# Performance work log

Measured on AMD Instinct MI355X. Metric: run time of the kernel, lower is better.

## Reference

```python
import jax, jax.numpy as jnp
import numpy as np

NUM_EXPERTS = 8
TOP_K = 2
HIDDEN = 1024
INTER_TOTAL = 8192  # intermediate_size * experts_per_rank
B, S = 2, 2048


def setup_inputs() -> dict:
    key = jax.random.key(0)
    k1, k2, k3, k4, k5, k6 = jax.random.split(key, 6)
    T = B * S
    x = jax.random.normal(k1, (B, S, HIDDEN), dtype=jnp.float32)
    scores = jax.random.uniform(k2, (T, NUM_EXPERTS), dtype=jnp.float32)
    expert_weights = jax.random.uniform(k3, (T, TOP_K), dtype=jnp.float32)
    top_experts = jax.random.randint(k4, (T, TOP_K), 0, NUM_EXPERTS, dtype=jnp.int32)
    w1 = jax.random.normal(k5, (HIDDEN, INTER_TOTAL), dtype=jnp.float32) * 0.02
    w2 = jax.random.normal(k6, (INTER_TOTAL, HIDDEN), dtype=jnp.float32) * 0.02
    return {"x": x, "scores": scores, "expert_weights": expert_weights,
            "top_experts": top_experts, "w1": w1, "w2": w2}


def reference(x, scores, expert_weights, top_experts, w1, w2):
    # forward_once with expert_parallel_size == 1 (dropless MoE dispatch/combine).
    in_shape = x.shape
    T = in_shape[0] * in_shape[1]
    H = in_shape[-1]
    x_flat = x.reshape(T, H)

    flat_experts = top_experts.reshape(-1)          # [T*top_k]
    flat_weights = expert_weights.reshape(-1)       # [T*top_k]

    # ops.sort: stable radix sort of routed copies by expert id
    order = jnp.argsort(flat_experts, stable=True)  # "indices"
    token_idx = order // TOP_K                      # source token per sorted slot

    # padded_gather: bucket tokens per expert (padding rows are zeros and
    # pass through the bias-free MLP as zeros, so they never affect output)
    xg = x_flat[token_idx]                          # [T*top_k, H]

    # MLP: w1 -> gelu(tanh approx) -> w2
    h = jax.nn.gelu(xg @ w1, approximate=True)      # [T*top_k, inter*E]
    y = h @ w2                                      # [T*top_k, H]

    # padded_scatter: weighted combine back to token order
    w_sorted = flat_weights[order]
    out = jnp.zeros((T, H), dtype=x.dtype).at[token_idx].add(w_sorted[:, None] * y)
    return out.reshape(in_shape)
```

## Files before the change

kernel.cpp:

```cpp
#include <hip/hip_runtime.h>
#include <hip/hip_bf16.h>
#include <math.h>

#define HID 1024
#define INTER 8192
#define TT 4096

typedef __bf16 bf16x8 __attribute__((ext_vector_type(8)));
typedef float f32x4 __attribute__((ext_vector_type(4)));

__device__ __forceinline__ void gll16(const void* g, void* l) {
    __builtin_amdgcn_global_load_lds(
        (const __attribute__((address_space(1))) void*)g,
        (__attribute__((address_space(3))) void*)l, 16, 0, 0);
}

__device__ __forceinline__ bf16x8 ds_read128(unsigned addr) {
    bf16x8 r;
    asm volatile("ds_read_b128 %0, %1" : "=v"(r) : "v"(addr));
    return r;
}

__global__ void k_prep(const float* __restrict__ x, const float* __restrict__ ew,
                       __hip_bfloat16* __restrict__ xb, float* __restrict__ s,
                       int n4, int T) {
    int stride = gridDim.x * blockDim.x;
    for (int i = blockIdx.x * blockDim.x + threadIdx.x; i < n4; i += stride) {
        float4 v = ((const float4*)x)[i];
        __hip_bfloat16* o = xb + (size_t)i * 4;
        o[0] = __float2bfloat16(v.x);
        o[1] = __float2bfloat16(v.y);
        o[2] = __float2bfloat16(v.z);
        o[3] = __float2bfloat16(v.w);
    }
    for (int t = blockIdx.x * blockDim.x + threadIdx.x; t < T; t += stride)
        s[t] = ew[2 * t] + ew[2 * t + 1];
}

__global__ void k_tcast(const float* __restrict__ in, __hip_bfloat16* __restrict__ out,
                        int R, int C) {
    __shared__ float tile[32][33];
    const int tx = threadIdx.x & 31, ty = threadIdx.x >> 5;
    const int br = blockIdx.y * 32, bc = blockIdx.x * 32;
#pragma unroll
    for (int j = 0; j < 32; j += 8)
        tile[ty + j][tx] = in[(size_t)(br + ty + j) * C + bc + tx];
    __syncthreads();
#pragma unroll
    for (int j = 0; j < 32; j += 8)
        out[(size_t)(bc + ty + j) * R + br + tx] = __float2bfloat16(tile[tx][ty + j]);
}

template <int EPI>
__global__ __launch_bounds__(512, 2) void k_gemm8(
    const __hip_bfloat16* __restrict__ A, const __hip_bfloat16* __restrict__ Bt,
    __hip_bfloat16* __restrict__ hOut, float* __restrict__ fOut,
    const float* __restrict__ s, int Kfull, int nt, int Nout) {
    __shared__ __hip_bfloat16 sA[2][2][128][64];
    __shared__ __hip_bfloat16 sB[2][2][128][64];
    const int tid = threadIdx.x;
    const int lane = tid & 63, wid = tid >> 6;
    const int wr = wid >> 2, wc = wid & 3;

    const int nwg = gridDim.x * gridDim.y;
    const int wg = blockIdx.y * gridDim.x + blockIdx.x;
    const int swz = (wg & 7) * (nwg >> 3) + (wg >> 3);
    const int brow = (swz / gridDim.x) * 256;
    const int bcol = (swz % gridDim.x) * 256;
    const size_t kbase = (size_t)blockIdx.z * ((size_t)nt * 64);

    const int colsw = (((lane & 7) ^ (lane >> 3)) << 3);
    const int qA0 = (wid & 3) * 4;
    const int bh = (wid >> 1) & 1;
    const int qB0 = ((wid & 1) | ((wid >> 2) << 1)) * 4;
    const __hip_bfloat16* gA2 =
        A + (size_t)(brow + wr * 128 + qA0 * 8 + (lane >> 3)) * Kfull + kbase + colsw;
    const __hip_bfloat16* gB2 =
        Bt + (size_t)(bcol + bh * 128 + qB0 * 8 + (lane >> 3)) * Kfull + kbase + colsw;
    char* ldsA2 = (char*)&sA[0][0][0][0] + wr * 16384 + qA0 * 1024;
    char* ldsB2 = (char*)&sB[0][0][0][0] + bh * 16384 + qB0 * 1024;
    const size_t chunkStep = (size_t)8 * Kfull;

    const unsigned baseA = (unsigned)(uintptr_t)&sA[0][0][0][0];
    const unsigned baseB = (unsigned)(uintptr_t)&sB[0][0][0][0];
    const unsigned g0 = (((lane >> 4)) ^ (lane & 7)) << 4;
    const unsigned g1 = ((4 + (lane >> 4)) ^ (lane & 7)) << 4;
    const unsigned rdA0 = baseA + wr * 16384 + (lane & 15) * 128 + g0;
    const unsigned rdA1 = baseA + wr * 16384 + (lane & 15) * 128 + g1;
    const unsigned rdB0 = baseB + (wc >> 1) * 16384 + (wc & 1) * 8192 + (lane & 15) * 128 + g0;
    const unsigned rdB1 = baseB + (wc >> 1) * 16384 + (wc & 1) * 8192 + (lane & 15) * 128 + g1;

    f32x4 acc[8][4] = {};
    bf16x8 aF[4][2], b01[2][2], b23[2][2];

#define STAGE_A2(buf, t)                                                       \
    do {                                                                       \
        _Pragma("unroll") for (int j = 0; j < 4; ++j)                          \
            gll16(gA2 + (size_t)j * chunkStep + (size_t)(t) * 64,              \
                  ldsA2 + (buf) * 32768 + j * 1024);                           \
    } while (0)
#define STAGE_B2(buf, t)                                                       \
    do {                                                                       \
        _Pragma("unroll") for (int j = 0; j < 4; ++j)                          \
            gll16(gB2 + (size_t)j * chunkStep + (size_t)(t) * 64,              \
                  ldsB2 + (buf) * 32768 + j * 1024);                           \
    } while (0)
#define PIN() __builtin_amdgcn_sched_barrier(0)
#define BAR()                              \
    do {                                   \
        PIN();                             \
        __builtin_amdgcn_s_barrier();      \
        PIN();                             \
    } while (0)
#define WAIT_LGKM0() __builtin_amdgcn_s_waitcnt(0xC07F)
#define WAIT_LGKM8() __builtin_amdgcn_s_waitcnt(0xC87F)
#define WAIT_VM0() __builtin_amdgcn_s_waitcnt(0x0F70)
#define RDA(buf, r, ks) ds_read128(((ks) ? rdA1 : rdA0) + (buf) * 32768u + (r) * 2048u)
#define RDB(buf, r, ks) ds_read128(((ks) ? rdB1 : rdB0) + (buf) * 32768u + (r) * 2048u)
#define MM_Q(mbase, nbase, bfr)                                                   \
    _Pragma("unroll") for (int ks = 0; ks < 2; ++ks)                              \
    _Pragma("unroll") for (int m = 0; m < 4; ++m)                                 \
    _Pragma("unroll") for (int n = 0; n < 2; ++n)                                 \
        acc[(mbase) + m][(nbase) + n] = __builtin_amdgcn_mfma_f32_16x16x32_bf16(  \
            aF[m][ks], bfr[n][ks], acc[(mbase) + m][(nbase) + n], 0, 0, 0);
#define MFMA_PHASE(mbase, nbase, bfr)     \
    do {                                  \
        WAIT_LGKM0();                     \
        PIN();                            \
        __builtin_amdgcn_s_setprio(1);    \
        MM_Q(mbase, nbase, bfr);          \
        __builtin_amdgcn_s_setprio(0);    \
        PIN();                            \
    } while (0)

    STAGE_A2(0, 0);
    STAGE_B2(0, 0);
    WAIT_VM0();
    BAR();

    const int iters = nt >> 1;
    for (int i = 0; i < iters; ++i) {
        const bool full = (i + 1 < iters);
        const int t1 = 2 * i + 1, t2 = 2 * i + 2;

#pragma unroll
        for (int m = 0; m < 4; ++m) {
            aF[m][0] = RDA(0, m, 0);
            aF[m][1] = RDA(0, m, 1);
        }
#pragma unroll
        for (int n = 0; n < 2; ++n) {
            b01[n][0] = RDB(0, n, 0);
            b01[n][1] = RDB(0, n, 1);
        }
        STAGE_A2(1, t1);
        WAIT_LGKM8();
        BAR();
        MFMA_PHASE(0, 0, b01);
        BAR();

#pragma unroll
        for (int n = 0; n < 2; ++n) {
            b23[n][0] = RDB(0, 2 + n, 0);
            b23[n][1] = RDB(0, 2 + n, 1);
        }
        STAGE_B2(1, t1);
        BAR();
        MFMA_PHASE(0, 2, b23);
        BAR();

#pragma unroll
        for (int m = 0; m < 4; ++m) {
            aF[m][0] = RDA(0, 4 + m, 0);
            aF[m][1] = RDA(0, 4 + m, 1);
        }
        BAR();
        MFMA_PHASE(4, 2, b23);
        BAR();

        BAR();
        MFMA_PHASE(4, 0, b01);
        WAIT_VM0();
        BAR();

#pragma unroll
        for (int m = 0; m < 4; ++m) {
            aF[m][0] = RDA(1, m, 0);
            aF[m][1] = RDA(1, m, 1);
        }
#pragma unroll
        for (int n = 0; n < 2; ++n) {
            b01[n][0] = RDB(1, n, 0);
            b01[n][1] = RDB(1, n, 1);
        }
        if (full) STAGE_A2(0, t2);
        WAIT_LGKM8();
        BAR();
        MFMA_PHASE(0, 0, b01);
        BAR();

#pragma unroll
        for (int n = 0; n < 2; ++n) {
            b23[n][0] = RDB(1, 2 + n, 0);
            b23[n][1] = RDB(1, 2 + n, 1);
        }
        if (full) STAGE_B2(0, t2);
        BAR();
        MFMA_PHASE(0, 2, b23);
        BAR();

#pragma unroll
        for (int m = 0; m < 4; ++m) {
            aF[m][0] = RDA(1, 4 + m, 0);
            aF[m][1] = RDA(1, 4 + m, 1);
        }
        BAR();
        MFMA_PHASE(4, 2, b23);
        BAR();

        BAR();
        MFMA_PHASE(4, 0, b01);
        WAIT_VM0();
        BAR();
    }

    const int orow = brow + wr * 128 + ((lane >> 4) << 2);
    const int ocol = bcol + wc * 64 + (lane & 15);
#pragma unroll
    for (int m = 0; m < 8; ++m) {
#pragma unroll
        for (int j = 0; j < 4; ++j) {
            const int r = orow + m * 16 + j;
            const size_t ro = (size_t)r * Nout;
            if (EPI == 0) {
#pragma unroll
                for (int n = 0; n < 4; ++n) {
                    float v = acc[m][n][j];
                    float u = 1.5957691216057308f * (v + 0.044715f * v * v * v);
                    float g = v / (1.0f + __expf(-u));
                    hOut[ro + ocol + n * 16] = __float2bfloat16(g);
                }
            } else {
                const float sc = s[r];
#pragma unroll
                for (int n = 0; n < 4; ++n)
                    unsafeAtomicAdd(&fOut[ro + ocol + n * 16], sc * acc[m][n][j]);
            }
        }
    }
#undef STAGE_A2
#undef STAGE_B2
#undef PIN
#undef BAR
#undef WAIT_LGKM0
#undef WAIT_LGKM8
#undef WAIT_VM0
#undef RDA
#undef RDB
#undef MM_Q
#undef MFMA_PHASE
}

extern "C" void kernel_launch(void* const* d_in, const int* in_sizes, int n_in,
                              void* d_out, int out_size, void* d_ws, size_t ws_size,
                              hipStream_t stream) {
    const float* x = (const float*)d_in[0];
    const float* ew = (const float*)d_in[2];
    const float* w1 = (const float*)d_in[4];
    const float* w2 = (const float*)d_in[5];
    float* out = (float*)d_out;

    char* ws = (char*)d_ws;
    float* s = (float*)ws;
    __hip_bfloat16* xb = (__hip_bfloat16*)(ws + 16384);
    __hip_bfloat16* w1t = (__hip_bfloat16*)(ws + 16384 + 8388608);
    __hip_bfloat16* w2t = (__hip_bfloat16*)(ws + 16384 + 8388608 + 16777216);
    __hip_bfloat16* h = (__hip_bfloat16*)(ws + 16384 + 8388608 + 2 * 16777216);

    k_prep<<<1024, 256, 0, stream>>>(x, ew, xb, s, (TT * HID) / 4, TT);

    dim3 t1(INTER / 32, HID / 32);
    k_tcast<<<t1, 256, 0, stream>>>(w1, w1t, HID, INTER);
    dim3 t2(HID / 32, INTER / 32);
    k_tcast<<<t2, 256, 0, stream>>>(w2, w2t, INTER, HID);

    dim3 g1(INTER / 256, TT / 256, 1);
    k_gemm8<0><<<g1, 512, 0, stream>>>(xb, w1t, h, nullptr, nullptr, HID, HID / 64, INTER);

    hipMemsetAsync(out, 0, (size_t)TT * HID * sizeof(float), stream);
    dim3 g2(HID / 256, TT / 256, 4);
    k_gemm8<1><<<g2, 512, 0, stream>>>(h, w2t, nullptr, out, s, INTER, 2048 / 64, HID);
}
```

Measured before the change: 211.3 us.

## Restructure GEMM main loop to one barrier per K-tile with bulk LDS reads

Replaces the 8-phase ping-pong main loop, which had many block barriers per pair of K-tiles, with a single-tile loop. Each iteration issues all 24 LDS fragment reads up front using immediate offsets, starts the next tile's global-to-LDS loads, and then runs four MFMA groups gated by partial lgkmcnt waits, ending with one barrier. The goal is to cut barrier and synchronisation overhead and overlap LDS reads with MFMAs. In exchange it holds more fragment registers live (a03 and a47 together), which raises VGPR pressure under the 512-thread, 2-block launch bound, and gives less interleaving between LDS reads and MFMAs inside an iteration.

New measurement: 202.5 us. 4.2% less time.

```diff
diff --git a/kernel.cpp b/kernel.cpp
--- a/kernel.cpp
+++ b/kernel.cpp
@@ -15,9 +15,10 @@
         (__attribute__((address_space(3))) void*)l, 16, 0, 0);
 }
 
-__device__ __forceinline__ bf16x8 ds_read128(unsigned addr) {
+template <int OFF>
+__device__ __forceinline__ bf16x8 ds_read128o(unsigned addr) {
     bf16x8 r;
-    asm volatile("ds_read_b128 %0, %1" : "=v"(r) : "v"(addr));
+    asm volatile("ds_read_b128 %0, %1 offset:%c2" : "=v"(r) : "v"(addr), "i"(OFF));
     return r;
 }
 
@@ -52,7 +53,7 @@
 }
 
 template <int EPI>
-__global__ __launch_bounds__(512, 2) void k_gemm8(
+__global__ __launch_bounds__(512, 2) void k_gemm1b(
     const __hip_bfloat16* __restrict__ A, const __hip_bfloat16* __restrict__ Bt,
     __hip_bfloat16* __restrict__ hOut, float* __restrict__ fOut,
     const float* __restrict__ s, int Kfull, int nt, int Nout) {
@@ -91,19 +92,19 @@
     const unsigned rdB1 = baseB + (wc >> 1) * 16384 + (wc & 1) * 8192 + (lane & 15) * 128 + g1;
 
     f32x4 acc[8][4] = {};
-    bf16x8 aF[4][2], b01[2][2], b23[2][2];
-
-#define STAGE_A2(buf, t)                                                       \
+    bf16x8 a03[4][2], a47[4][2], b01[2][2], b23[2][2];
+
+#define STAGE_A2(bufoff, t)                                                    \
     do {                                                                       \
         _Pragma("unroll") for (int j = 0; j < 4; ++j)                          \
             gll16(gA2 + (size_t)j * chunkStep + (size_t)(t) * 64,              \
-                  ldsA2 + (buf) * 32768 + j * 1024);                           \
+                  ldsA2 + (bufoff) + j * 1024);                                \
     } while (0)
-#define STAGE_B2(buf, t)                                                       \
+#define STAGE_B2(bufoff, t)                                                    \
     do {                                                                       \
         _Pragma("unroll") for (int j = 0; j < 4; ++j)                          \
             gll16(gB2 + (size_t)j * chunkStep + (size_t)(t) * 64,              \
-                  ldsB2 + (buf) * 32768 + j * 1024);                           \
+                  ldsB2 + (bufoff) + j * 1024);                                \
     } while (0)
 #define PIN() __builtin_amdgcn_sched_barrier(0)
 #define BAR()                              \
@@ -112,114 +113,97 @@
         __builtin_amdgcn_s_barrier();      \
         PIN();                             \
     } while (0)
-#define WAIT_LGKM0() __builtin_amdgcn_s_waitcnt(0xC07F)
-#define WAIT_LGKM8() __builtin_amdgcn_s_waitcnt(0xC87F)
+#define WAIT_LG12() __builtin_amdgcn_s_waitcnt(0xCC7F)
+#define WAIT_LG8() __builtin_amdgcn_s_waitcnt(0xC87F)
+#define WAIT_LG0() __builtin_amdgcn_s_waitcnt(0xC07F)
 #define WAIT_VM0() __builtin_amdgcn_s_waitcnt(0x0F70)
-#define RDA(buf, r, ks) ds_read128(((ks) ? rdA1 : rdA0) + (buf) * 32768u + (r) * 2048u)
-#define RDB(buf, r, ks) ds_read128(((ks) ? rdB1 : rdB0) + (buf) * 32768u + (r) * 2048u)
-#define MM_Q(mbase, nbase, bfr)                                                   \
-    _Pragma("unroll") for (int ks = 0; ks < 2; ++ks)                              \
-    _Pragma("unroll") for (int m = 0; m < 4; ++m)                                 \
-    _Pragma("unroll") for (int n = 0; n < 2; ++n)                                 \
-        acc[(mbase) + m][(nbase) + n] = __builtin_amdgcn_mfma_f32_16x16x32_bf16(  \
-            aF[m][ks], bfr[n][ks], acc[(mbase) + m][(nbase) + n], 0, 0, 0);
-#define MFMA_PHASE(mbase, nbase, bfr)     \
-    do {                                  \
-        WAIT_LGKM0();                     \
-        PIN();                            \
-        __builtin_amdgcn_s_setprio(1);    \
-        MM_Q(mbase, nbase, bfr);          \
-        __builtin_amdgcn_s_setprio(0);    \
-        PIN();                            \
-    } while (0)
-
-    STAGE_A2(0, 0);
-    STAGE_B2(0, 0);
+
+    STAGE_A2(0u, 0);
+    STAGE_B2(0u, 0);
     WAIT_VM0();
     BAR();
 
-    const int iters = nt >> 1;
-    for (int i = 0; i < iters; ++i) {
-        const bool full = (i + 1 < iters);
-        const int t1 = 2 * i + 1, t2 = 2 * i + 2;
-
-#pragma unroll
-        for (int m = 0; m < 4; ++m) {
-            aF[m][0] = RDA(0, m, 0);
-            aF[m][1] = RDA(0, m, 1);
+#pragma unroll 1
+    for (int i = 0; i < nt; ++i) {
+        const unsigned co = (i & 1) ? 32768u : 0u;
+        const unsigned no = co ^ 32768u;
+        const bool full = (i + 1 < nt);
+        const unsigned aA0 = rdA0 + co, aA1 = rdA1 + co;
+        const unsigned aB0 = rdB0 + co, aB1 = rdB1 + co;
+
+        a03[0][0] = ds_read128o<0>(aA0);
+        a03[0][1] = ds_read128o<0>(aA1);
+        a03[1][0] = ds_read128o<2048>(aA0);
+        a03[1][1] = ds_read128o<2048>(aA1);
+        a03[2][0] = ds_read128o<4096>(aA0);
+        a03[2][1] = ds_read128o<4096>(aA1);
+        a03[3][0] = ds_read128o<6144>(aA0);
+        a03[3][1] = ds_read128o<6144>(aA1);
+        b01[0][0] = ds_read128o<0>(aB0);
+        b01[0][1] = ds_read128o<0>(aB1);
+        b01[1][0] = ds_read128o<2048>(aB0);
+        b01[1][1] = ds_read128o<2048>(aB1);
+        b23[0][0] = ds_read128o<4096>(aB0);
+        b23[0][1] = ds_read128o<4096>(aB1);
+        b23[1][0] = ds_read128o<6144>(aB0);
+        b23[1][1] = ds_read128o<6144>(aB1);
+        a47[0][0] = ds_read128o<8192>(aA0);
+        a47[0][1] = ds_read128o<8192>(aA1);
+        a47[1][0] = ds_read128o<10240>(aA0);
+        a47[1][1] = ds_read128o<10240>(aA1);
+        a47[2][0] = ds_read128o<12288>(aA0);
+        a47[2][1] = ds_read128o<12288>(aA1);
+        a47[3][0] = ds_read128o<14336>(aA0);
+        a47[3][1] = ds_read128o<14336>(aA1);
+
+        if (full) {
+            STAGE_A2(no, i + 1);
+            STAGE_B2(no, i + 1);
         }
-#pragma unroll
-        for (int n = 0; n < 2; ++n) {
-            b01[n][0] = RDB(0, n, 0);
-            b01[n][1] = RDB(0, n, 1);
-        }
-        STAGE_A2(1, t1);
-        WAIT_LGKM8();
-        BAR();
-        MFMA_PHASE(0, 0, b01);
-        BAR();
-
-#pragma unroll
-        for (int n = 0; n < 2; ++n) {
-            b23[n][0] = RDB(0, 2 + n, 0);
-            b23[n][1] = RDB(0, 2 + n, 1);
-        }
-        STAGE_B2(1, t1);
-        BAR();
-        MFMA_PHASE(0, 2, b23);
-        BAR();
-
-#pragma unroll
-        for (int m = 0; m < 4; ++m) {
-            aF[m][0] = RDA(0, 4 + m, 0);
-            aF[m][1] = RDA(0, 4 + m, 1);
-        }
-        BAR();
-        MFMA_PHASE(4, 2, b23);
-        BAR();
-
-        BAR();
-        MFMA_PHASE(4, 0, b01);
-        WAIT_VM0();
-        BAR();
-
-#pragma unroll
-        for (int m = 0; m < 4; ++m) {
-            aF[m][0] = RDA(1, m, 0);
-            aF[m][1] = RDA(1, m, 1);
-        }
-#pragma unroll
-        for (int n = 0; n < 2; ++n) {
-            b01[n][0] = RDB(1, n, 0);
-            b01[n][1] = RDB(1, n, 1);
-        }
-        if (full) STAGE_A2(0, t2);
-        WAIT_LGKM8();
-        BAR();
-        MFMA_PHASE(0, 0, b01);
-        BAR();
-
-#pragma unroll
-        for (int n = 0; n < 2; ++n) {
-            b23[n][0] = RDB(1, 2 + n, 0);
-            b23[n][1] = RDB(1, 2 + n, 1);
-        }
-        if (full) STAGE_B2(0, t2);
-        BAR();
-        MFMA_PHASE(0, 2, b23);
-        BAR();
-
-#pragma unroll
-        for (int m = 0; m < 4; ++m) {
-            aF[m][0] = RDA(1, 4 + m, 0);
-            aF[m][1] = RDA(1, 4 + m, 1);
-        }
-        BAR();
-        MFMA_PHASE(4, 2, b23);
-        BAR();
-
-        BAR();
-        MFMA_PHASE(4, 0, b01);
+
+        __builtin_amdgcn_s_setprio(1);
+        WAIT_LG12();
+        PIN();
+#pragma unroll
+        for (int ks = 0; ks < 2; ++ks)
+#pragma unroll
+            for (int m = 0; m < 4; ++m)
+#pragma unroll
+                for (int n = 0; n < 2; ++n)
+                    acc[m][n] = __builtin_amdgcn_mfma_f32_16x16x32_bf16(
+                        a03[m][ks], b01[n][ks], acc[m][n], 0, 0, 0);
+        PIN();
+        WAIT_LG8();
+        PIN();
+#pragma unroll
+        for (int ks = 0; ks < 2; ++ks)
+#pragma unroll
+            for (int m = 0; m < 4; ++m)
+#pragma unroll
+                for (int n = 0; n < 2; ++n)
+                    acc[m][2 + n] = __builtin_amdgcn_mfma_f32_16x16x32_bf16(
+                        a03[m][ks], b23[n][ks], acc[m][2 + n], 0, 0, 0);
+        PIN();
+        WAIT_LG0();
+        PIN();
+#pragma unroll
+        for (int ks = 0; ks < 2; ++ks)
+#pragma unroll
+            for (int m = 0; m < 4; ++m)
+#pragma unroll
+                for (int n = 0; n < 2; ++n)
+                    acc[4 + m][2 + n] = __builtin_amdgcn_mfma_f32_16x16x32_bf16(
+                        a47[m][ks], b23[n][ks], acc[4 + m][2 + n], 0, 0, 0);
+#pragma unroll
+        for (int ks = 0; ks < 2; ++ks)
+#pragma unroll
+            for (int m = 0; m < 4; ++m)
+#pragma unroll
+                for (int n = 0; n < 2; ++n)
+                    acc[4 + m][n] = __builtin_amdgcn_mfma_f32_16x16x32_bf16(
+                        a47[m][ks], b01[n][ks], acc[4 + m][n], 0, 0, 0);
+        __builtin_amdgcn_s_setprio(0);
+        PIN();
         WAIT_VM0();
         BAR();
     }
@@ -252,13 +236,10 @@
 #undef STAGE_B2
 #undef PIN
 #undef BAR
-#undef WAIT_LGKM0
-#undef WAIT_LGKM8
+#undef WAIT_LG12
+#undef WAIT_LG8
+#undef WAIT_LG0
 #undef WAIT_VM0
-#undef RDA
-#undef RDB
-#undef MM_Q
-#undef MFMA_PHASE
 }
 
 extern "C" void kernel_launch(void* const* d_in, const int* in_sizes, int n_in,
@@ -285,9 +266,9 @@
     k_tcast<<<t2, 256, 0, stream>>>(w2, w2t, INTER, HID);
 
     dim3 g1(INTER / 256, TT / 256, 1);
-    k_gemm8<0><<<g1, 512, 0, stream>>>(xb, w1t, h, nullptr, nullptr, HID, HID / 64, INTER);
+    k_gemm1b<0><<<g1, 512, 0, stream>>>(xb, w1t, h, nullptr, nullptr, HID, HID / 64, INTER);
 
     hipMemsetAsync(out, 0, (size_t)TT * HID * sizeof(float), stream);
     dim3 g2(HID / 256, TT / 256, 4);
-    k_gemm8<1><<<g2, 512, 0, stream>>>(h, w2t, nullptr, out, s, INTER, 2048 / 64, HID);
-}
+    k_gemm1b<1><<<g2, 512, 0, stream>>>(h, w2t, nullptr, out, s, INTER, 2048 / 64, HID);
+}
```
